# Performance work log

Measured on AMD Instinct MI355X. Metric: run time of the kernel, lower is better.

Reference implementation:

```python
import jax, jax.numpy as jnp
import numpy as np

B, CTRL, KEY, MEMU = 64, 512, 64, 16384  # batch, controller_size, key_size(=memory_unit_size), memory_units
EPS_COS = 1e-8   # torch F.cosine_similarity default eps
EPS_NORM = 1e-16


def setup_inputs() -> dict:
    key = jax.random.key(0)
    ks = jax.random.split(key, 16)
    controller_state = jax.random.normal(ks[0], (B, CTRL), jnp.float32)
    pw = jax.random.uniform(ks[1], (B, MEMU), jnp.float32)
    prev_weights = pw / jnp.sum(pw, axis=1, keepdims=True)  # valid attention weights
    memory = jax.random.normal(ks[2], (B, MEMU, KEY), jnp.float32)
    def lin(k, out_d, in_d):
        kw, kb = jax.random.split(k)
        scale = 1.0 / np.sqrt(in_d)
        return (jax.random.normal(kw, (out_d, in_d), jnp.float32) * scale,
                jax.random.normal(kb, (out_d,), jnp.float32) * 0.01)
    key_W, key_b = lin(ks[3], KEY, CTRL)
    ks_W, ks_b = lin(ks[4], 1, CTRL)
    ig_W, ig_b = lin(ks[5], 1, CTRL)
    sw_W, sw_b = lin(ks[6], 3, CTRL)
    sf_W, sf_b = lin(ks[7], 1, CTRL)
    wd_W, wd_b = lin(ks[8], KEY, CTRL)
    return dict(controller_state=controller_state, prev_weights=prev_weights, memory=memory,
                key_W=key_W, key_b=key_b, ks_W=ks_W, ks_b=ks_b, ig_W=ig_W, ig_b=ig_b,
                sw_W=sw_W, sw_b=sw_b, sf_W=sf_W, sf_b=sf_b, wd_W=wd_W, wd_b=wd_b)


def _ntm_head(cs, prev_w, mem, key_W, key_b, ks_W, ks_b, ig_W, ig_b, sw_W, sw_b, sf_W, sf_b, wd_W, wd_b):
    k = cs @ key_W.T + key_b                       # (B, KEY)
    b = jax.nn.softplus(cs @ ks_W.T + ks_b)        # (B, 1) key strength
    g = jax.nn.sigmoid(cs @ ig_W.T + ig_b)         # (B, 1) interpolation gate
    s = jax.nn.softmax(cs @ sw_W.T + sw_b, axis=-1)  # (B, 3) shift weights
    y = 1.0 + jax.nn.softplus(cs @ sf_W.T + sf_b)  # (B, 1) sharpen factor
    # content addressing: softmax(b * cosine_sim(key, memory rows))
    dots = jnp.einsum('bmw,bw->bm', mem, k)        # (B, MEMU)
    denom = jnp.maximum(jnp.linalg.norm(mem, axis=2) * jnp.linalg.norm(k, axis=1, keepdims=True), EPS_COS)
    w_c = jax.nn.softmax(b * (dots / denom), axis=1)
    # interpolation with previous weights
    w_i = g * w_c + (1.0 - g) * prev_w             # (B, MEMU)
    # 3-tap circular shift (cross-correlation, matching the padded conv1d)
    shifted = (s[:, 0:1] * jnp.roll(w_i, 1, axis=1)
               + s[:, 1:2] * w_i
               + s[:, 2:3] * jnp.roll(w_i, -1, axis=1))
    # sharpen + normalize
    sharp = shifted ** y
    w = sharp / (jnp.sum(sharp, axis=1, keepdims=True) + EPS_NORM)
    data = jnp.einsum('bm,bmw->bw', w, mem)        # read mode
    return w, data


def reference(controller_state, prev_weights, memory, key_W, key_b, ks_W, ks_b,
              ig_W, ig_b, sw_W, sw_b, sf_W, sf_b, wd_W, wd_b):
    return _ntm_head(controller_state, prev_weights, memory, key_W, key_b, ks_W, ks_b,
                     ig_W, ig_b, sw_W, sw_b, sf_W, sf_b, wd_W, wd_b)
```

## Files before the change

kernel.cpp:

```cpp
#include <hip/hip_runtime.h>
#include <math.h>

#define B    64
#define CTRL 512
#define KEY  64
#define MEMU 16384

__device__ __forceinline__ float softplusf(float x) {
    return x > 20.f ? x : log1pf(expf(x));
}

__global__ __launch_bounds__(256) void k1_scalars(
    const float* __restrict__ cs,
    const float* __restrict__ key_W, const float* __restrict__ key_b,
    const float* __restrict__ ks_W,  const float* __restrict__ ks_b,
    const float* __restrict__ ig_W,  const float* __restrict__ ig_b,
    const float* __restrict__ sw_W,  const float* __restrict__ sw_b,
    const float* __restrict__ sf_W,  const float* __restrict__ sf_b,
    float* __restrict__ ws_k, float* __restrict__ ws_scal)
{
    __shared__ float cs_s[CTRL];
    __shared__ float k_s[KEY];
    __shared__ float h_s[8];
    const int b = blockIdx.x;
    const int t = threadIdx.x;
    for (int i = t; i < CTRL; i += 256) cs_s[i] = cs[b * CTRL + i];
    __syncthreads();
    const int wave = t >> 6, lane = t & 63;
    for (int o = wave; o < 70; o += 4) {
        const float* W; float bias;
        if (o < 64)       { W = key_W + o * CTRL;      bias = key_b[o]; }
        else if (o == 64) { W = ks_W;                  bias = ks_b[0]; }
        else if (o == 65) { W = ig_W;                  bias = ig_b[0]; }
        else if (o < 69)  { W = sw_W + (o - 66) * CTRL; bias = sw_b[o - 66]; }
        else              { W = sf_W;                  bias = sf_b[0]; }
        float d = 0.f;
        for (int j = lane; j < CTRL; j += 64) d += cs_s[j] * W[j];
        #pragma unroll
        for (int off = 32; off >= 1; off >>= 1) d += __shfl_xor(d, off, 64);
        if (lane == 0) {
            float r = d + bias;
            if (o < 64) { k_s[o] = r; ws_k[b * KEY + o] = r; }
            else        h_s[o - 64] = r;
        }
    }
    __syncthreads();
    if (wave == 0) {
        float kv = k_s[lane];
        float sq = kv * kv;
        #pragma unroll
        for (int off = 32; off >= 1; off >>= 1) sq += __shfl_xor(sq, off, 64);
        if (lane == 0) {
            float knorm = sqrtf(sq);
            float beta = softplusf(h_s[0]);
            float g    = 1.f / (1.f + expf(-h_s[1]));
            float m3   = fmaxf(fmaxf(h_s[2], h_s[3]), h_s[4]);
            float e0 = expf(h_s[2] - m3), e1 = expf(h_s[3] - m3), e2 = expf(h_s[4] - m3);
            float inv3 = 1.f / (e0 + e1 + e2);
            float y = 1.f + softplusf(h_s[5]);
            float* sc = ws_scal + b * 8;
            sc[0] = beta; sc[1] = g;
            sc[2] = e0 * inv3; sc[3] = e1 * inv3; sc[4] = e2 * inv3;
            sc[5] = y; sc[6] = knorm;
        }
    }
}

__global__ __launch_bounds__(256) void k2_scores(
    const float* __restrict__ mem,
    const float* __restrict__ ws_k, const float* __restrict__ ws_scal,
    float* __restrict__ ws_e, float* __restrict__ ws_pe)
{
    const int b = blockIdx.y;
    const int chunk = blockIdx.x;
    const int t = threadIdx.x;
    const float beta  = ws_scal[b * 8 + 0];
    const float knorm = ws_scal[b * 8 + 6];
    float kk[KEY];
    #pragma unroll
    for (int j = 0; j < KEY; ++j) kk[j] = ws_k[b * KEY + j];

    float esum = 0.f;
    #pragma unroll
    for (int i = 0; i < 4; ++i) {
        const int m = chunk * 1024 + i * 256 + t;
        const float4* rp = (const float4*)(mem + ((size_t)b * MEMU + m) * KEY);
        float dot = 0.f, sq = 0.f;
        #pragma unroll
        for (int q = 0; q < 16; ++q) {
            float4 v = rp[q];
            dot += v.x * kk[4*q+0] + v.y * kk[4*q+1] + v.z * kk[4*q+2] + v.w * kk[4*q+3];
            sq  += v.x * v.x + v.y * v.y + v.z * v.z + v.w * v.w;
        }
        const float denom = fmaxf(sqrtf(sq) * knorm, 1e-8f);
        const float e = expf(beta * (dot / denom) - beta);
        ws_e[b * MEMU + m] = e;
        esum += e;
    }
    __shared__ float red[4];
    #pragma unroll
    for (int off = 32; off >= 1; off >>= 1) esum += __shfl_xor(esum, off, 64);
    if ((t & 63) == 0) red[t >> 6] = esum;
    __syncthreads();
    if (t == 0) ws_pe[b * 16 + chunk] = red[0] + red[1] + red[2] + red[3];
}

__global__ __launch_bounds__(256) void k4_sharp(
    const float* __restrict__ pw,
    const float* __restrict__ ws_e, const float* __restrict__ ws_pe,
    const float* __restrict__ ws_scal,
    float* __restrict__ ws_sharp, float* __restrict__ ws_ps)
{
    const int b = blockIdx.y, chunk = blockIdx.x, t = threadIdx.x;
    float sum_e = 0.f;
    #pragma unroll
    for (int i = 0; i < 16; ++i) sum_e += ws_pe[b * 16 + i];
    const float inv_e = 1.f / sum_e;
    const float g  = ws_scal[b*8+1];
    const float s0 = ws_scal[b*8+2], s1 = ws_scal[b*8+3], s2 = ws_scal[b*8+4];
    const float y  = ws_scal[b*8+5];
    const float cg = 1.f - g;
    const float* eb = ws_e + b * MEMU;
    const float* pb = pw   + b * MEMU;

    float ssum = 0.f;
    #pragma unroll
    for (int i = 0; i < 8; ++i) {
        const int m  = chunk * 2048 + i * 256 + t;
        const int mm = (m + MEMU - 1) & (MEMU - 1);
        const int mp = (m + 1) & (MEMU - 1);
        const float wim = g * eb[mm] * inv_e + cg * pb[mm];
        const float wi0 = g * eb[m ] * inv_e + cg * pb[m ];
        const float wip = g * eb[mp] * inv_e + cg * pb[mp];
        const float sh  = s0 * wim + s1 * wi0 + s2 * wip;
        const float sp  = expf(y * logf(sh));
        ws_sharp[b * MEMU + m] = sp;
        ssum += sp;
    }
    __shared__ float red[4];
    #pragma unroll
    for (int off = 32; off >= 1; off >>= 1) ssum += __shfl_xor(ssum, off, 64);
    if ((t & 63) == 0) red[t >> 6] = ssum;
    __syncthreads();
    if (t == 0) ws_ps[b * 8 + chunk] = red[0] + red[1] + red[2] + red[3];
}

__global__ __launch_bounds__(256) void k7_data(
    const float* __restrict__ mem,
    const float* __restrict__ ws_sharp, const float* __restrict__ ws_ps,
    float* __restrict__ out_w, float* __restrict__ ws_pd)
{
    const int b     = (B - 1) - blockIdx.y;
    const int chunk = 63 - blockIdx.x;
    const int t = threadIdx.x, wv = t >> 6, lane = t & 63;
    __shared__ float w_lds[256];
    __shared__ float red[4][64];

    float ss = 0.f;
    #pragma unroll
    for (int i = 0; i < 8; ++i) ss += ws_ps[b * 8 + i];
    const float inv = 1.f / (ss + 1e-16f);

    const int m0 = chunk * 256;
    const float wval = ws_sharp[b * MEMU + m0 + t] * inv;
    __builtin_nontemporal_store(wval, &out_w[b * MEMU + m0 + t]);
    w_lds[t] = wval;
    __syncthreads();

    const float* mb = mem + ((size_t)b * MEMU + m0 + wv * 64) * KEY;
    const int rsub = lane >> 4;
    const int c4   = (lane & 15) * 4;
    float4 acc = make_float4(0.f, 0.f, 0.f, 0.f);
    #pragma unroll
    for (int s = 0; s < 16; ++s) {
        const int r = s * 4 + rsub;
        const float4 v = *(const float4*)(mb + (size_t)r * KEY + c4);
        const float wr = w_lds[wv * 64 + r];
        acc.x += wr * v.x; acc.y += wr * v.y; acc.z += wr * v.z; acc.w += wr * v.w;
    }
    #pragma unroll
    for (int off = 16; off <= 32; off <<= 1) {
        acc.x += __shfl_xor(acc.x, off, 64);
        acc.y += __shfl_xor(acc.y, off, 64);
        acc.z += __shfl_xor(acc.z, off, 64);
        acc.w += __shfl_xor(acc.w, off, 64);
    }
    if (lane < 16) {
        red[wv][c4 + 0] = acc.x; red[wv][c4 + 1] = acc.y;
        red[wv][c4 + 2] = acc.z; red[wv][c4 + 3] = acc.w;
    }
    __syncthreads();
    if (t < 64) {
        ws_pd[(b * 64 + chunk) * 64 + t] =
            red[0][t] + red[1][t] + red[2][t] + red[3][t];
    }
}

__global__ __launch_bounds__(64) void k8_reduce(
    const float* __restrict__ ws_pd, float* __restrict__ out)
{
    const int b = blockIdx.x, j = threadIdx.x;
    float s = 0.f;
    #pragma unroll 8
    for (int c = 0; c < 64; ++c) s += ws_pd[(b * 64 + c) * 64 + j];
    out[(size_t)B * MEMU + b * KEY + j] = s;
}

extern "C" void kernel_launch(void* const* d_in, const int* in_sizes, int n_in,
                              void* d_out, int out_size, void* d_ws, size_t ws_size,
                              hipStream_t stream) {
    (void)in_sizes; (void)n_in; (void)out_size; (void)ws_size;
    const float* cs    = (const float*)d_in[0];
    const float* pw    = (const float*)d_in[1];
    const float* mem   = (const float*)d_in[2];
    const float* key_W = (const float*)d_in[3];
    const float* key_b = (const float*)d_in[4];
    const float* ks_W  = (const float*)d_in[5];
    const float* ks_b  = (const float*)d_in[6];
    const float* ig_W  = (const float*)d_in[7];
    const float* ig_b  = (const float*)d_in[8];
    const float* sw_W  = (const float*)d_in[9];
    const float* sw_b  = (const float*)d_in[10];
    const float* sf_W  = (const float*)d_in[11];
    const float* sf_b  = (const float*)d_in[12];
    float* out = (float*)d_out;
    float* ws  = (float*)d_ws;

    float* ws_k     = ws;
    float* ws_scal  = ws_k + B * KEY;
    float* ws_e     = ws_scal + B * 8;
    float* ws_sharp = ws_e + (size_t)B * MEMU;
    float* ws_pe    = ws_sharp + (size_t)B * MEMU;
    float* ws_ps    = ws_pe + B * 16;
    float* ws_pd    = ws_ps + B * 8;

    k1_scalars<<<dim3(B), dim3(256), 0, stream>>>(cs, key_W, key_b, ks_W, ks_b,
                                                  ig_W, ig_b, sw_W, sw_b, sf_W, sf_b,
                                                  ws_k, ws_scal);
    k2_scores<<<dim3(16, B), dim3(256), 0, stream>>>(mem, ws_k, ws_scal, ws_e, ws_pe);
    k4_sharp<<<dim3(8, B), dim3(256), 0, stream>>>(pw, ws_e, ws_pe, ws_scal, ws_sharp, ws_ps);
    k7_data<<<dim3(64, B), dim3(256), 0, stream>>>(mem, ws_sharp, ws_ps, out, ws_pd);
    k8_reduce<<<dim3(B), dim3(64), 0, stream>>>(ws_pd, out);
}
```

Before: 118.9 us.

## Coalesce memory reads in score kernel, vectorize sharpen loads, widen final reduce

The score kernel previously had each thread read a full 256-byte memory row, so a wavefront's loads were strided. Now each row is split across 16 lanes, each reading a float4 so a wavefront reads contiguous rows, and dot products and squared norms are combined with shuffles. The sharpen kernel gives each thread 8 contiguous elements loaded as float4 plus two halo values, removing the redundant neighbour loads, and stores with float4. The final reduce uses 256 threads with an LDS combine. The trade-off is extra shuffle work per row and only one lane in 16 doing the exp and store.

```diff
diff --git a/kernel.cpp b/kernel.cpp
--- a/kernel.cpp
+++ b/kernel.cpp
@@ -73,34 +73,38 @@
 {
     const int b = blockIdx.y;
     const int chunk = blockIdx.x;
-    const int t = threadIdx.x;
+    const int t = threadIdx.x, wv = t >> 6, lane = t & 63;
     const float beta  = ws_scal[b * 8 + 0];
     const float knorm = ws_scal[b * 8 + 6];
-    float kk[KEY];
-    #pragma unroll
-    for (int j = 0; j < KEY; ++j) kk[j] = ws_k[b * KEY + j];
-
+    const int c4   = (lane & 15) * 4;
+    const int rsub = lane >> 4;
+    const float4 kv = *(const float4*)(ws_k + b * KEY + c4);
+
+    const int R0 = chunk * 1024 + wv * 256;
+    const float* mb = mem + ((size_t)b * MEMU + R0) * KEY;
     float esum = 0.f;
-    #pragma unroll
-    for (int i = 0; i < 4; ++i) {
-        const int m = chunk * 1024 + i * 256 + t;
-        const float4* rp = (const float4*)(mem + ((size_t)b * MEMU + m) * KEY);
-        float dot = 0.f, sq = 0.f;
+    #pragma unroll 8
+    for (int s = 0; s < 64; ++s) {
+        const int r = s * 4 + rsub;
+        const float4 v = *(const float4*)(mb + (size_t)r * KEY + c4);
+        float dot = v.x * kv.x + v.y * kv.y + v.z * kv.z + v.w * kv.w;
+        float sq  = v.x * v.x + v.y * v.y + v.z * v.z + v.w * v.w;
         #pragma unroll
-        for (int q = 0; q < 16; ++q) {
-            float4 v = rp[q];
-            dot += v.x * kk[4*q+0] + v.y * kk[4*q+1] + v.z * kk[4*q+2] + v.w * kk[4*q+3];
-            sq  += v.x * v.x + v.y * v.y + v.z * v.z + v.w * v.w;
-        }
-        const float denom = fmaxf(sqrtf(sq) * knorm, 1e-8f);
-        const float e = expf(beta * (dot / denom) - beta);
-        ws_e[b * MEMU + m] = e;
-        esum += e;
-    }
+        for (int off = 1; off <= 8; off <<= 1) {
+            dot += __shfl_xor(dot, off, 64);
+            sq  += __shfl_xor(sq,  off, 64);
+        }
+        if ((lane & 15) == 0) {
+            const float denom = fmaxf(sqrtf(sq) * knorm, 1e-8f);
+            const float e = expf(beta * (dot / denom) - beta);
+            ws_e[b * MEMU + R0 + r] = e;
+            esum += e;
+        }
+    }
+    esum += __shfl_xor(esum, 16, 64);
+    esum += __shfl_xor(esum, 32, 64);
     __shared__ float red[4];
-    #pragma unroll
-    for (int off = 32; off >= 1; off >>= 1) esum += __shfl_xor(esum, off, 64);
-    if ((t & 63) == 0) red[t >> 6] = esum;
+    if (lane == 0) red[wv] = esum;
     __syncthreads();
     if (t == 0) ws_pe[b * 16 + chunk] = red[0] + red[1] + red[2] + red[3];
 }
@@ -123,20 +127,39 @@
     const float* eb = ws_e + b * MEMU;
     const float* pb = pw   + b * MEMU;
 
+    const int m = chunk * 2048 + t * 8;
+    const float4 e0 = *(const float4*)(eb + m);
+    const float4 e1 = *(const float4*)(eb + m + 4);
+    const float  el = eb[(m + MEMU - 1) & (MEMU - 1)];
+    const float  er = eb[(m + 8) & (MEMU - 1)];
+    const float4 p0 = *(const float4*)(pb + m);
+    const float4 p1 = *(const float4*)(pb + m + 4);
+    const float  pl = pb[(m + MEMU - 1) & (MEMU - 1)];
+    const float  pr = pb[(m + 8) & (MEMU - 1)];
+
+    float wi[10];
+    wi[0] = g * el   * inv_e + cg * pl;
+    wi[1] = g * e0.x * inv_e + cg * p0.x;
+    wi[2] = g * e0.y * inv_e + cg * p0.y;
+    wi[3] = g * e0.z * inv_e + cg * p0.z;
+    wi[4] = g * e0.w * inv_e + cg * p0.w;
+    wi[5] = g * e1.x * inv_e + cg * p1.x;
+    wi[6] = g * e1.y * inv_e + cg * p1.y;
+    wi[7] = g * e1.z * inv_e + cg * p1.z;
+    wi[8] = g * e1.w * inv_e + cg * p1.w;
+    wi[9] = g * er   * inv_e + cg * pr;
+
+    float sp[8];
     float ssum = 0.f;
     #pragma unroll
-    for (int i = 0; i < 8; ++i) {
-        const int m  = chunk * 2048 + i * 256 + t;
-        const int mm = (m + MEMU - 1) & (MEMU - 1);
-        const int mp = (m + 1) & (MEMU - 1);
-        const float wim = g * eb[mm] * inv_e + cg * pb[mm];
-        const float wi0 = g * eb[m ] * inv_e + cg * pb[m ];
-        const float wip = g * eb[mp] * inv_e + cg * pb[mp];
-        const float sh  = s0 * wim + s1 * wi0 + s2 * wip;
-        const float sp  = expf(y * logf(sh));
-        ws_sharp[b * MEMU + m] = sp;
-        ssum += sp;
-    }
+    for (int k = 0; k < 8; ++k) {
+        const float sh = s0 * wi[k] + s1 * wi[k+1] + s2 * wi[k+2];
+        sp[k] = expf(y * logf(sh));
+        ssum += sp[k];
+    }
+    *(float4*)(ws_sharp + b * MEMU + m)     = make_float4(sp[0], sp[1], sp[2], sp[3]);
+    *(float4*)(ws_sharp + b * MEMU + m + 4) = make_float4(sp[4], sp[5], sp[6], sp[7]);
+
     __shared__ float red[4];
     #pragma unroll
     for (int off = 32; off >= 1; off >>= 1) ssum += __shfl_xor(ssum, off, 64);
@@ -196,14 +219,21 @@
     }
 }
 
-__global__ __launch_bounds__(64) void k8_reduce(
+__global__ __launch_bounds__(256) void k8_reduce(
     const float* __restrict__ ws_pd, float* __restrict__ out)
 {
-    const int b = blockIdx.x, j = threadIdx.x;
+    const int b = blockIdx.x, t = threadIdx.x;
+    const int j = t & 63, cg = t >> 6;
+    const float* pd = ws_pd + b * 4096;
     float s = 0.f;
-    #pragma unroll 8
-    for (int c = 0; c < 64; ++c) s += ws_pd[(b * 64 + c) * 64 + j];
-    out[(size_t)B * MEMU + b * KEY + j] = s;
+    #pragma unroll
+    for (int c = cg; c < 64; c += 4) s += pd[c * 64 + j];
+    __shared__ float red[4][64];
+    red[cg][j] = s;
+    __syncthreads();
+    if (t < 64)
+        out[(size_t)B * MEMU + b * KEY + t] =
+            red[0][t] + red[1][t] + red[2][t] + red[3][t];
 }
 
 extern "C" void kernel_launch(void* const* d_in, const int* in_sizes, int n_in,
@@ -240,5 +270,5 @@
     k2_scores<<<dim3(16, B), dim3(256), 0, stream>>>(mem, ws_k, ws_scal, ws_e, ws_pe);
     k4_sharp<<<dim3(8, B), dim3(256), 0, stream>>>(pw, ws_e, ws_pe, ws_scal, ws_sharp, ws_ps);
     k7_data<<<dim3(64, B), dim3(256), 0, stream>>>(mem, ws_sharp, ws_ps, out, ws_pd);
-    k8_reduce<<<dim3(B), dim3(64), 0, stream>>>(ws_pd, out);
-}
+    k8_reduce<<<dim3(B), dim3(256), 0, stream>>>(ws_pd, out);
+}
```

After: 129.6 us. 9.0% more time.

## Fuse sharpen into read kernel and defer normalization to final pass

Applied to the files above, without the earlier changes.

Merges the sharpen kernel into the memory-read kernel so each block computes unnormalized sharpened weights for its 256 rows, stores them to the output and uses them directly for the weighted read. Normalization by the global sum is deferred to a final kernel that rescales both the read vector and the weight output. This removes one launch and the round trip of the sharpened weights through the workspace. In exchange the weight output is rewritten in place, and each final block redundantly sums 64 partial sums.

```diff
diff --git a/kernel.cpp b/kernel.cpp
--- a/kernel.cpp
+++ b/kernel.cpp
@@ -105,13 +105,20 @@
     if (t == 0) ws_pe[b * 16 + chunk] = red[0] + red[1] + red[2] + red[3];
 }
 
-__global__ __launch_bounds__(256) void k4_sharp(
-    const float* __restrict__ pw,
+__global__ __launch_bounds__(256) void kC_data(
+    const float* __restrict__ mem, const float* __restrict__ pw,
     const float* __restrict__ ws_e, const float* __restrict__ ws_pe,
     const float* __restrict__ ws_scal,
-    float* __restrict__ ws_sharp, float* __restrict__ ws_ps)
-{
-    const int b = blockIdx.y, chunk = blockIdx.x, t = threadIdx.x;
+    float* __restrict__ out_w, float* __restrict__ ws_pd,
+    float* __restrict__ ws_ps)
+{
+    const int b     = (B - 1) - blockIdx.y;
+    const int chunk = 63 - blockIdx.x;
+    const int t = threadIdx.x, wv = t >> 6, lane = t & 63;
+    __shared__ float w_lds[256];
+    __shared__ float red[4][64];
+    __shared__ float red1[4];
+
     float sum_e = 0.f;
     #pragma unroll
     for (int i = 0; i < 16; ++i) sum_e += ws_pe[b * 16 + i];
@@ -120,52 +127,27 @@
     const float s0 = ws_scal[b*8+2], s1 = ws_scal[b*8+3], s2 = ws_scal[b*8+4];
     const float y  = ws_scal[b*8+5];
     const float cg = 1.f - g;
+
+    const int m0 = chunk * 256;
+    const int m  = m0 + t;
+    const int mm = (m + MEMU - 1) & (MEMU - 1);
+    const int mp = (m + 1) & (MEMU - 1);
     const float* eb = ws_e + b * MEMU;
     const float* pb = pw   + b * MEMU;
-
-    float ssum = 0.f;
-    #pragma unroll
-    for (int i = 0; i < 8; ++i) {
-        const int m  = chunk * 2048 + i * 256 + t;
-        const int mm = (m + MEMU - 1) & (MEMU - 1);
-        const int mp = (m + 1) & (MEMU - 1);
-        const float wim = g * eb[mm] * inv_e + cg * pb[mm];
-        const float wi0 = g * eb[m ] * inv_e + cg * pb[m ];
-        const float wip = g * eb[mp] * inv_e + cg * pb[mp];
-        const float sh  = s0 * wim + s1 * wi0 + s2 * wip;
-        const float sp  = expf(y * logf(sh));
-        ws_sharp[b * MEMU + m] = sp;
-        ssum += sp;
-    }
-    __shared__ float red[4];
+    const float wim = g * eb[mm] * inv_e + cg * pb[mm];
+    const float wi0 = g * eb[m ] * inv_e + cg * pb[m ];
+    const float wip = g * eb[mp] * inv_e + cg * pb[mp];
+    const float sh  = s0 * wim + s1 * wi0 + s2 * wip;
+    const float sp  = expf(y * logf(sh));
+    out_w[b * MEMU + m] = sp;
+    w_lds[t] = sp;
+
+    float ssum = sp;
     #pragma unroll
     for (int off = 32; off >= 1; off >>= 1) ssum += __shfl_xor(ssum, off, 64);
-    if ((t & 63) == 0) red[t >> 6] = ssum;
-    __syncthreads();
-    if (t == 0) ws_ps[b * 8 + chunk] = red[0] + red[1] + red[2] + red[3];
-}
-
-__global__ __launch_bounds__(256) void k7_data(
-    const float* __restrict__ mem,
-    const float* __restrict__ ws_sharp, const float* __restrict__ ws_ps,
-    float* __restrict__ out_w, float* __restrict__ ws_pd)
-{
-    const int b     = (B - 1) - blockIdx.y;
-    const int chunk = 63 - blockIdx.x;
-    const int t = threadIdx.x, wv = t >> 6, lane = t & 63;
-    __shared__ float w_lds[256];
-    __shared__ float red[4][64];
-
-    float ss = 0.f;
-    #pragma unroll
-    for (int i = 0; i < 8; ++i) ss += ws_ps[b * 8 + i];
-    const float inv = 1.f / (ss + 1e-16f);
-
-    const int m0 = chunk * 256;
-    const float wval = ws_sharp[b * MEMU + m0 + t] * inv;
-    __builtin_nontemporal_store(wval, &out_w[b * MEMU + m0 + t]);
-    w_lds[t] = wval;
-    __syncthreads();
+    if (lane == 0) red1[wv] = ssum;
+    __syncthreads();
+    if (t == 0) ws_ps[b * 64 + chunk] = red1[0] + red1[1] + red1[2] + red1[3];
 
     const float* mb = mem + ((size_t)b * MEMU + m0 + wv * 64) * KEY;
     const int rsub = lane >> 4;
@@ -196,14 +178,43 @@
     }
 }
 
-__global__ __launch_bounds__(64) void k8_reduce(
-    const float* __restrict__ ws_pd, float* __restrict__ out)
-{
-    const int b = blockIdx.x, j = threadIdx.x;
-    float s = 0.f;
-    #pragma unroll 8
-    for (int c = 0; c < 64; ++c) s += ws_pd[(b * 64 + c) * 64 + j];
-    out[(size_t)B * MEMU + b * KEY + j] = s;
+__global__ __launch_bounds__(256) void kD_final(
+    const float* __restrict__ ws_pd, const float* __restrict__ ws_ps,
+    float* __restrict__ out)
+{
+    const int bid = blockIdx.x, t = threadIdx.x;
+    if (bid < B) {
+        const int b = bid;
+        float S = 0.f;
+        #pragma unroll
+        for (int c = 0; c < 64; ++c) S += ws_ps[b * 64 + c];
+        const float inv = 1.f / (S + 1e-16f);
+        const int j = t & 63, g4 = t >> 6;
+        const float* pd = ws_pd + b * 4096;
+        float s = 0.f;
+        #pragma unroll
+        for (int c = g4; c < 64; c += 4) s += pd[c * 64 + j];
+        __shared__ float red[4][64];
+        red[g4][j] = s;
+        __syncthreads();
+        if (t < 64)
+            out[(size_t)B * MEMU + b * KEY + t] =
+                (red[0][t] + red[1][t] + red[2][t] + red[3][t]) * inv;
+    } else {
+        const int u = bid - B;
+        const int b = u >> 3, seg = u & 7;
+        float S = 0.f;
+        #pragma unroll
+        for (int c = 0; c < 64; ++c) S += ws_ps[b * 64 + c];
+        const float inv = 1.f / (S + 1e-16f);
+        float* wbase = out + (size_t)b * MEMU + seg * 2048 + t * 8;
+        float4 a0 = *(float4*)wbase;
+        float4 a1 = *(float4*)(wbase + 4);
+        a0.x *= inv; a0.y *= inv; a0.z *= inv; a0.w *= inv;
+        a1.x *= inv; a1.y *= inv; a1.z *= inv; a1.w *= inv;
+        *(float4*)wbase       = a0;
+        *(float4*)(wbase + 4) = a1;
+    }
 }
 
 extern "C" void kernel_launch(void* const* d_in, const int* in_sizes, int n_in,
@@ -226,19 +237,18 @@
     float* out = (float*)d_out;
     float* ws  = (float*)d_ws;
 
-    float* ws_k     = ws;
-    float* ws_scal  = ws_k + B * KEY;
-    float* ws_e     = ws_scal + B * 8;
-    float* ws_sharp = ws_e + (size_t)B * MEMU;
-    float* ws_pe    = ws_sharp + (size_t)B * MEMU;
-    float* ws_ps    = ws_pe + B * 16;
-    float* ws_pd    = ws_ps + B * 8;
+    float* ws_k    = ws;
+    float* ws_scal = ws_k + B * KEY;
+    float* ws_e    = ws_scal + B * 8;
+    float* ws_pe   = ws_e + (size_t)B * MEMU;
+    float* ws_ps   = ws_pe + B * 16;
+    float* ws_pd   = ws_ps + B * 64;
 
     k1_scalars<<<dim3(B), dim3(256), 0, stream>>>(cs, key_W, key_b, ks_W, ks_b,
                                                   ig_W, ig_b, sw_W, sw_b, sf_W, sf_b,
                                                   ws_k, ws_scal);
     k2_scores<<<dim3(16, B), dim3(256), 0, stream>>>(mem, ws_k, ws_scal, ws_e, ws_pe);
-    k4_sharp<<<dim3(8, B), dim3(256), 0, stream>>>(pw, ws_e, ws_pe, ws_scal, ws_sharp, ws_ps);
-    k7_data<<<dim3(64, B), dim3(256), 0, stream>>>(mem, ws_sharp, ws_ps, out, ws_pd);
-    k8_reduce<<<dim3(B), dim3(64), 0, stream>>>(ws_pd, out);
-}
+    kC_data<<<dim3(64, B), dim3(256), 0, stream>>>(mem, pw, ws_e, ws_pe, ws_scal,
+                                                   out, ws_pd, ws_ps);
+    kD_final<<<dim3(B + 512), dim3(256), 0, stream>>>(ws_pd, ws_ps, out);
+}
```

Result: no change. 118.1 us (-0.7%).
